# Kernel tuning notes

Measured on AMD Instinct MI355X. Metric: run time of the kernel, lower is better.

## Reference

```python
import jax, jax.numpy as jnp
import numpy as np

INPUT_DIM = 768
OUTPUT_DIM = 768
GRID_SIZE = 5
BATCH = 8192


def setup_inputs() -> dict:
    key = jax.random.key(0)
    k1, k2 = jax.random.split(key)
    x = jax.random.normal(k1, (BATCH, INPUT_DIM), dtype=jnp.float32)
    coeffs = jax.random.normal(k2, (INPUT_DIM, OUTPUT_DIM, GRID_SIZE), dtype=jnp.float32) * 0.1
    scale = jnp.ones((INPUT_DIM, OUTPUT_DIM), dtype=jnp.float32)
    shift = jnp.zeros((INPUT_DIM, OUTPUT_DIM), dtype=jnp.float32)
    return {"x": x, "coeffs": coeffs, "scale": scale, "shift": shift}


def reference(x, coeffs, scale, shift):
    # x: [B, I]; coeffs: [I, J, G]; scale/shift: [I, J]
    grid = jnp.linspace(-1.0, 1.0, GRID_SIZE, dtype=x.dtype)        # [G]
    x_norm = jnp.tanh(x)                                            # [B, I]
    # RBF basis: exp(-5 * (x_norm - grid)^2) -> [B, I, G]
    basis = jnp.exp(-5.0 * (x_norm[:, :, None] - grid) ** 2)
    # Fold scale into coeffs, contract over input dim and grid:
    # out[b,j] = sum_{i,g} basis[b,i,g] * coeffs[i,j,g] * scale[i,j] + sum_i shift[i,j]
    w = coeffs * scale[:, :, None]                                  # [I, J, G]
    out = jnp.einsum('big,ijg->bj', basis, w)                       # [B, J]
    out = out + jnp.sum(shift, axis=0)                              # broadcast bias [J]
    return out
```

## Files before the change

### kernel.cpp

```cpp
#include <hip/hip_runtime.h>
#include <hip/hip_bf16.h>
#include <cstdint>
#include <cstddef>

#define BATCH 8192
#define IDIM  768
#define JDIM  768
#define GRID  5
#define KDIM  (IDIM * GRID)


__device__ __forceinline__ unsigned short f2bf(float f) {
    unsigned int u = __float_as_uint(f);
    u += 0x7fffu + ((u >> 16) & 1u);
    return (unsigned short)(u >> 16);
}

typedef __bf16 bf16x8 __attribute__((ext_vector_type(8)));
typedef float  f32x4  __attribute__((ext_vector_type(4)));
typedef unsigned short ushortx4 __attribute__((ext_vector_type(4)));

__device__ __forceinline__ void async_copy16(const void* gsrc, void* ldsdst) {
    __builtin_amdgcn_global_load_lds(
        (const __attribute__((address_space(1))) unsigned int*)gsrc,
        (__attribute__((address_space(3))) unsigned int*)ldsdst,
        16, 0, 0);
}


#define WT_I 32
#define WT_J 64

__global__ __launch_bounds__(256)
void wt_bias_kernel(const float* __restrict__ coeffs,
                    const float* __restrict__ scale,
                    const float* __restrict__ shift,
                    unsigned short* __restrict__ Wt,
                    float* __restrict__ bias) {
    __shared__ __align__(16) unsigned short tile[GRID][WT_J][WT_I + 4];
    __shared__ float red[4][WT_J];
    const int t  = threadIdx.x;
    const int i0 = (blockIdx.x / (JDIM / WT_J)) * WT_I;
    const int j0 = (blockIdx.x % (JDIM / WT_J)) * WT_J;
    const int jj = t & 63;

    float ssum = 0.f;
#pragma unroll
    for (int it = 0; it < (WT_I * WT_J) / 256; ++it) {
        const int ii = it * 4 + (t >> 6);
        const int i = i0 + ii, j = j0 + jj;
        const float* cp = &coeffs[((size_t)i * JDIM + j) * GRID];
        const float  sc = scale[(size_t)i * JDIM + j];
        ssum += shift[(size_t)i * JDIM + j];
#pragma unroll
        for (int g = 0; g < GRID; ++g)
            tile[g][jj][ii] = f2bf(cp[g] * sc);
    }
    red[t >> 6][jj] = ssum;
    __syncthreads();
    if (t < WT_J)
        atomicAdd(&bias[j0 + t], red[0][t] + red[1][t] + red[2][t] + red[3][t]);

#pragma unroll
    for (int it = 0; it < (WT_J * GRID * (WT_I / 4)) / 256; ++it) {
        const int p  = it * 256 + t;
        const int iq = p & 7;
        const int q  = p >> 3;
        const int g  = q % GRID;
        const int j  = q / GRID;
        ushortx4 v = *(const ushortx4*)&tile[g][j][iq * 4];
        *(ushortx4*)&Wt[(size_t)(j0 + j) * KDIM + g * IDIM + i0 + iq * 4] = v;
    }
}


__global__ __launch_bounds__(256)
void basis_kernel(const float* __restrict__ x, unsigned short* __restrict__ Abas) {
    const int idx = blockIdx.x * 256 + threadIdx.x;
    const int b  = idx / (IDIM / 4);
    const int i4 = (idx - b * (IDIM / 4)) * 4;
    const float4 xv = *(const float4*)&x[(size_t)b * IDIM + i4];
    const float xs[4] = {xv.x, xv.y, xv.z, xv.w};
    float tv[4];
#pragma unroll
    for (int u = 0; u < 4; ++u) {
        const float e = __expf(2.f * xs[u]);
        tv[u] = 1.f - 2.f / (e + 1.f);
    }
#pragma unroll
    for (int g = 0; g < GRID; ++g) {
        const float gv = -1.f + 0.5f * (float)g;
        ushortx4 o;
#pragma unroll
        for (int u = 0; u < 4; ++u) {
            const float d = tv[u] - gv;
            o[u] = f2bf(__expf(-5.f * d * d));
        }
        *(ushortx4*)&Abas[(size_t)b * KDIM + g * IDIM + i4] = o;
    }
}


#define BM 128
#define BN 96
#define BK 64

__global__ __launch_bounds__(256, 2)
void kan_gemm(const unsigned short* __restrict__ Abas,
              const unsigned short* __restrict__ Wt,
              const float* __restrict__ bias,
              float* __restrict__ out) {
    __shared__ unsigned short As[2][BM * BK];
    __shared__ unsigned short Bs[2][BN * BK];

    const int t    = threadIdx.x;
    const int lane = t & 63;
    const int wave = t >> 6;
    const int m0 = blockIdx.x * BM;
    const int n0 = blockIdx.y * BN;
    const int wm = (wave >> 1) * 64;
    const int wn = (wave & 1) * 48;

    f32x4 acc[4][3] = {};

    const int lrow = t >> 3;
    const int lc   = t & 7;
    const int cg   = lc ^ (lrow & 7);
    const int ldsoff = lrow * BK + lc * 8;
    const size_t abase = (size_t)(m0 + lrow) * KDIM + cg * 8;
    const size_t bbase = (size_t)(n0 + lrow) * KDIM + cg * 8;

#pragma unroll
    for (int s = 0; s < 4; ++s)
        async_copy16(&Abas[abase + (size_t)(32 * s) * KDIM], &As[0][ldsoff + 32 * s * BK]);
#pragma unroll
    for (int s = 0; s < 3; ++s)
        async_copy16(&Wt[bbase + (size_t)(32 * s) * KDIM], &Bs[0][ldsoff + 32 * s * BK]);
    asm volatile("s_waitcnt vmcnt(0)" ::: "memory");
    __syncthreads();

    int cur = 0;
    for (int kt = 0; kt < KDIM; kt += BK) {
        const int nxt = cur ^ 1;
        if (kt + BK < KDIM) {
#pragma unroll
            for (int s = 0; s < 4; ++s)
                async_copy16(&Abas[abase + (size_t)(32 * s) * KDIM + kt + BK],
                             &As[nxt][ldsoff + 32 * s * BK]);
#pragma unroll
            for (int s = 0; s < 3; ++s)
                async_copy16(&Wt[bbase + (size_t)(32 * s) * KDIM + kt + BK],
                             &Bs[nxt][ldsoff + 32 * s * BK]);
        }

#pragma unroll
        for (int ks = 0; ks < 2; ++ks) {
            const int pc = ((ks * 4) + (lane >> 4)) ^ (lane & 7);
            bf16x8 af[4], bfr[3];
#pragma unroll
            for (int f = 0; f < 4; ++f)
                af[f]  = *(const bf16x8*)&As[cur][(wm + f * 16 + (lane & 15)) * BK + pc * 8];
#pragma unroll
            for (int f = 0; f < 3; ++f)
                bfr[f] = *(const bf16x8*)&Bs[cur][(wn + f * 16 + (lane & 15)) * BK + pc * 8];
#pragma unroll
            for (int fm = 0; fm < 4; ++fm)
#pragma unroll
                for (int fn = 0; fn < 3; ++fn)
                    acc[fm][fn] = __builtin_amdgcn_mfma_f32_16x16x32_bf16(
                        af[fm], bfr[fn], acc[fm][fn], 0, 0, 0);
        }

        asm volatile("s_waitcnt vmcnt(0)" ::: "memory");
        __syncthreads();
        cur = nxt;
    }

    const int col   = lane & 15;
    const int rbase = (lane >> 4) * 4;
#pragma unroll
    for (int fm = 0; fm < 4; ++fm) {
#pragma unroll
        for (int fn = 0; fn < 3; ++fn) {
            const int j  = n0 + wn + fn * 16 + col;
            const float bj = bias[j];
#pragma unroll
            for (int r = 0; r < 4; ++r) {
                const int row = m0 + wm + fm * 16 + rbase + r;
                out[(size_t)row * JDIM + j] = acc[fm][fn][r] + bj;
            }
        }
    }
}


__global__ __launch_bounds__(256)
void fallback_kernel(const float* __restrict__ x,
                     const float* __restrict__ coeffs,
                     const float* __restrict__ scale,
                     const float* __restrict__ shift,
                     float* __restrict__ out) {
    __shared__ float bas[KDIM];
    const int b = blockIdx.x;
    const int t = threadIdx.x;
    for (int i = t; i < IDIM; i += 256) {
        float tv = tanhf(x[(size_t)b * IDIM + i]);
#pragma unroll
        for (int g = 0; g < GRID; ++g) {
            float d = tv - (-1.0f + 0.5f * (float)g);
            bas[g * IDIM + i] = __expf(-5.0f * d * d);
        }
    }
    __syncthreads();
#pragma unroll
    for (int jj = 0; jj < 3; ++jj) {
        const int j = t + jj * 256;
        float acc = 0.f;
        for (int i = 0; i < IDIM; ++i) {
            const float sc = scale[(size_t)i * JDIM + j];
            const float* cp = &coeffs[((size_t)i * JDIM + j) * GRID];
            float s5 = 0.f;
#pragma unroll
            for (int g = 0; g < GRID; ++g) s5 += bas[g * IDIM + i] * cp[g];
            acc += s5 * sc + shift[(size_t)i * JDIM + j];
        }
        out[(size_t)b * JDIM + j] = acc;
    }
}


extern "C" void kernel_launch(void* const* d_in, const int* in_sizes, int n_in,
                              void* d_out, int out_size, void* d_ws, size_t ws_size,
                              hipStream_t stream) {
    const float* x      = (const float*)d_in[0];
    const float* coeffs = (const float*)d_in[1];
    const float* scale  = (const float*)d_in[2];
    const float* shift  = (const float*)d_in[3];
    float* out = (float*)d_out;

    const size_t wt_bytes   = (size_t)JDIM * KDIM * sizeof(unsigned short);
    const size_t bias_off   = wt_bytes;
    const size_t bias_bytes = (size_t)JDIM * sizeof(float);
    const size_t bas_off    = bias_off + bias_bytes;
    const size_t bas_bytes  = (size_t)BATCH * KDIM * sizeof(unsigned short);
    const size_t need       = bas_off + bas_bytes;

    if (ws_size >= need) {
        unsigned short* Wt   = (unsigned short*)d_ws;
        float*          bias = (float*)((char*)d_ws + bias_off);
        unsigned short* Abas = (unsigned short*)((char*)d_ws + bas_off);

        hipMemsetAsync(bias, 0, bias_bytes, stream);
        wt_bias_kernel<<<(IDIM / WT_I) * (JDIM / WT_J), 256, 0, stream>>>(coeffs, scale, shift, Wt, bias);
        basis_kernel<<<(BATCH * (IDIM / 4)) / 256, 256, 0, stream>>>(x, Abas);
        kan_gemm<<<dim3(BATCH / BM, JDIM / BN), 256, 0, stream>>>(Abas, Wt, bias, out);
    } else {
        fallback_kernel<<<BATCH, 256, 0, stream>>>(x, coeffs, scale, shift, out);
    }
}
```

Before: 163.2 us.

## Triple-buffer A tiles and use partial vmcnt waits in GEMM mainloop

Restructures the GEMM K-loop so A tiles are prefetched two stages ahead into a third LDS buffer while B stays double-buffered. The loop now waits only for older loads with partial vmcnt counts and uses raw s_barrier plus sched_barrier instead of a full drain each iteration, with explicit epilogue iterations. The aim is to hide more global-load latency behind MFMA work. In exchange it uses more LDS, which may reduce occupancy below two blocks per CU, and the hand-counted vmcnt values must match the exact number of outstanding loads.

```diff
diff --git a/kernel.cpp b/kernel.cpp
--- a/kernel.cpp
+++ b/kernel.cpp
@@ -104,13 +104,14 @@
 #define BM 128
 #define BN 96
 #define BK 64
+#define KT (KDIM / BK)
 
 __global__ __launch_bounds__(256, 2)
 void kan_gemm(const unsigned short* __restrict__ Abas,
               const unsigned short* __restrict__ Wt,
               const float* __restrict__ bias,
               float* __restrict__ out) {
-    __shared__ unsigned short As[2][BM * BK];
+    __shared__ unsigned short As[3][BM * BK];
     __shared__ unsigned short Bs[2][BN * BK];
 
     const int t    = threadIdx.x;
@@ -130,39 +131,30 @@
     const size_t abase = (size_t)(m0 + lrow) * KDIM + cg * 8;
     const size_t bbase = (size_t)(n0 + lrow) * KDIM + cg * 8;
 
-#pragma unroll
-    for (int s = 0; s < 4; ++s)
-        async_copy16(&Abas[abase + (size_t)(32 * s) * KDIM], &As[0][ldsoff + 32 * s * BK]);
-#pragma unroll
-    for (int s = 0; s < 3; ++s)
-        async_copy16(&Wt[bbase + (size_t)(32 * s) * KDIM], &Bs[0][ldsoff + 32 * s * BK]);
-    asm volatile("s_waitcnt vmcnt(0)" ::: "memory");
-    __syncthreads();
-
-    int cur = 0;
-    for (int kt = 0; kt < KDIM; kt += BK) {
-        const int nxt = cur ^ 1;
-        if (kt + BK < KDIM) {
-#pragma unroll
-            for (int s = 0; s < 4; ++s)
-                async_copy16(&Abas[abase + (size_t)(32 * s) * KDIM + kt + BK],
-                             &As[nxt][ldsoff + 32 * s * BK]);
-#pragma unroll
-            for (int s = 0; s < 3; ++s)
-                async_copy16(&Wt[bbase + (size_t)(32 * s) * KDIM + kt + BK],
-                             &Bs[nxt][ldsoff + 32 * s * BK]);
-        }
-
+    auto stage_a = [&](int buf, int kt_el) {
+#pragma unroll
+        for (int s = 0; s < 4; ++s)
+            async_copy16(&Abas[abase + (size_t)(32 * s) * KDIM + kt_el],
+                         &As[buf][ldsoff + 32 * s * BK]);
+    };
+    auto stage_b = [&](int buf, int kt_el) {
+#pragma unroll
+        for (int s = 0; s < 3; ++s)
+            async_copy16(&Wt[bbase + (size_t)(32 * s) * KDIM + kt_el],
+                         &Bs[buf][ldsoff + 32 * s * BK]);
+    };
+
+    auto compute_tile = [&](int ab, int bb) {
 #pragma unroll
         for (int ks = 0; ks < 2; ++ks) {
             const int pc = ((ks * 4) + (lane >> 4)) ^ (lane & 7);
             bf16x8 af[4], bfr[3];
 #pragma unroll
             for (int f = 0; f < 4; ++f)
-                af[f]  = *(const bf16x8*)&As[cur][(wm + f * 16 + (lane & 15)) * BK + pc * 8];
+                af[f]  = *(const bf16x8*)&As[ab][(wm + f * 16 + (lane & 15)) * BK + pc * 8];
 #pragma unroll
             for (int f = 0; f < 3; ++f)
-                bfr[f] = *(const bf16x8*)&Bs[cur][(wn + f * 16 + (lane & 15)) * BK + pc * 8];
+                bfr[f] = *(const bf16x8*)&Bs[bb][(wn + f * 16 + (lane & 15)) * BK + pc * 8];
 #pragma unroll
             for (int fm = 0; fm < 4; ++fm)
 #pragma unroll
@@ -170,10 +162,40 @@
                     acc[fm][fn] = __builtin_amdgcn_mfma_f32_16x16x32_bf16(
                         af[fm], bfr[fn], acc[fm][fn], 0, 0, 0);
         }
-
+    };
+
+    stage_a(0, 0);
+    stage_a(1, BK);
+    stage_b(0, 0);
+
+    int ac = 0, a2 = 2;
+    for (int tt = 0; tt < KT - 2; ++tt) {
+        stage_a(a2, (tt + 2) * BK);
+        stage_b((tt + 1) & 1, (tt + 1) * BK);
+        asm volatile("s_waitcnt vmcnt(7)" ::: "memory");
+        __builtin_amdgcn_s_barrier();
+        __builtin_amdgcn_sched_barrier(0);
+        compute_tile(ac, tt & 1);
+        __builtin_amdgcn_s_barrier();
+        ac = (ac == 2) ? 0 : ac + 1;
+        a2 = (a2 == 2) ? 0 : a2 + 1;
+    }
+    {
+        const int tt = KT - 2;
+        stage_b((tt + 1) & 1, (tt + 1) * BK);
+        asm volatile("s_waitcnt vmcnt(3)" ::: "memory");
+        __builtin_amdgcn_s_barrier();
+        __builtin_amdgcn_sched_barrier(0);
+        compute_tile(ac, tt & 1);
+        __builtin_amdgcn_s_barrier();
+        ac = (ac == 2) ? 0 : ac + 1;
+    }
+    {
+        const int tt = KT - 1;
         asm volatile("s_waitcnt vmcnt(0)" ::: "memory");
-        __syncthreads();
-        cur = nxt;
+        __builtin_amdgcn_s_barrier();
+        __builtin_amdgcn_sched_barrier(0);
+        compute_tile(ac, tt & 1);
     }
 
     const int col   = lane & 15;
```

Result: faster. 157.3 us (-3.6%).
